# Performance work log

Measured on AMD Instinct MI355X. Metric: run time of the kernel, lower is better.

## Reference

```python
import jax, jax.numpy as jnp
import numpy as np

N_HEAD = 16
E = 1024
B, T = 2, 2048


def setup_inputs() -> dict:
    key = jax.random.key(0)
    ks = jax.random.split(key, 5)
    s = 1.0 / np.sqrt(E)
    return {
        "x": jax.random.normal(ks[0], (B, T, E), dtype=jnp.float32),
        "w_qkv": jax.random.normal(ks[1], (E, 3 * E), dtype=jnp.float32) * s,
        "b_qkv": jnp.zeros((3 * E,), dtype=jnp.float32),
        "w_proj": jax.random.normal(ks[2], (E, E), dtype=jnp.float32) * s,
        "b_proj": jnp.zeros((E,), dtype=jnp.float32),
    }


def reference(x, w_qkv, b_qkv, w_proj, b_proj):
    Bsz, Tlen, Emb = x.shape
    hd = Emb // N_HEAD
    qkv = x @ w_qkv + b_qkv  # [B, T, 3E]
    q, k, v = jnp.split(qkv, 3, axis=-1)
    # [B, H, T, hd]
    q = q.reshape(Bsz, Tlen, N_HEAD, hd).transpose(0, 2, 1, 3)
    k = k.reshape(Bsz, Tlen, N_HEAD, hd).transpose(0, 2, 1, 3)
    v = v.reshape(Bsz, Tlen, N_HEAD, hd).transpose(0, 2, 1, 3)
    scale = 1.0 / jnp.sqrt(jnp.asarray(hd, dtype=x.dtype))
    scores = jnp.einsum("bhqd,bhkd->bhqk", q, k) * scale  # [B, H, T, T]
    causal = jnp.tril(jnp.ones((Tlen, Tlen), dtype=bool))
    scores = jnp.where(causal, scores, jnp.asarray(-jnp.inf, dtype=scores.dtype))
    attn = jax.nn.softmax(scores, axis=-1)
    y = jnp.einsum("bhqk,bhkd->bhqd", attn, v)  # [B, H, T, hd]
    y = y.transpose(0, 2, 1, 3).reshape(Bsz, Tlen, Emb)
    return y @ w_proj + b_proj
```

## Files before the change

kernel.cpp:

```cpp
#include <hip/hip_runtime.h>
#include <hip/hip_bf16.h>

typedef __hip_bfloat16 bf16;
typedef __attribute__((ext_vector_type(8))) short sh8;
typedef __attribute__((ext_vector_type(4))) float f32x4;

#define BB 2
#define TT 2048
#define EE 1024
#define NH 16
#define HD 64
#define M_ROWS (BB * TT)
#define PPAD 72

__device__ __forceinline__ float b2f(bf16 v) { return __bfloat162float(v); }
__device__ __forceinline__ bf16 f2b(float v) { return __float2bfloat16(v); }
__device__ __forceinline__ unsigned short f2bu(float v) {
    union { bf16 b; unsigned short u; } x; x.b = f2b(v); return x.u;
}

__device__ __forceinline__ void gl2lds16(const bf16* g, bf16* l) {
    __builtin_amdgcn_global_load_lds(
        (__attribute__((address_space(1))) void*)g,
        (__attribute__((address_space(3))) void*)l, 16, 0, 0);
}

__global__ __launch_bounds__(256) void prep(
    const float* __restrict__ x, bf16* __restrict__ xb,
    const float* __restrict__ Wq, bf16* __restrict__ Wqt,
    const float* __restrict__ Wp, bf16* __restrict__ Wpt) {
    const int bid = blockIdx.x;
    if (bid < 4096) {
        const int i = bid * 256 + threadIdx.x;
        const float4 v = ((const float4*)x)[i];
        ushort4 u;
        u.x = f2bu(v.x); u.y = f2bu(v.y); u.z = f2bu(v.z); u.w = f2bu(v.w);
        ((ushort4*)xb)[i] = u;
        return;
    }
    __shared__ float Ld[64][65];
    const float* src; bf16* dst; int ncols, nc0, kr0;
    if (bid < 4096 + 768) {
        const int t = bid - 4096;
        src = Wq; dst = Wqt; ncols = 3072;
        nc0 = (t % 48) * 64; kr0 = (t / 48) * 64;
    } else {
        const int t = bid - 4096 - 768;
        src = Wp; dst = Wpt; ncols = 1024;
        nc0 = (t % 16) * 64; kr0 = (t / 16) * 64;
    }
#pragma unroll
    for (int i = 0; i < 16; ++i) {
        const int e = threadIdx.x + i * 256;
        Ld[e >> 6][e & 63] = src[(size_t)(kr0 + (e >> 6)) * ncols + nc0 + (e & 63)];
    }
    __syncthreads();
#pragma unroll
    for (int i = 0; i < 16; ++i) {
        const int e = threadIdx.x + i * 256;
        const int r2 = e & 63, c2 = e >> 6;
        dst[(size_t)(nc0 + c2) * EE + kr0 + r2] = f2b(Ld[r2][c2]);
    }
}

__device__ __forceinline__ void mfma_gemm_core(
    const bf16* __restrict__ A, const bf16* __restrict__ Bt,
    int m0, int n0, f32x4 acc[4][4], bf16* Al, bf16* Bl) {
    const int tid = threadIdx.x, w = tid >> 6, lane = tid & 63;
    const int li = lane & 15, quad = lane >> 4;
    const int wm = (w & 1) * 64, wn = (w >> 1) * 64;
    const int srow = w * 32 + (lane >> 3);
    const int scol = (lane & 7) * 8;

#pragma unroll
    for (int mt = 0; mt < 4; ++mt)
#pragma unroll
        for (int nt = 0; nt < 4; ++nt) acc[mt][nt] = (f32x4){0.f, 0.f, 0.f, 0.f};

    for (int k0 = 0; k0 < EE; k0 += 64) {
        __syncthreads();
#pragma unroll
        for (int j = 0; j < 4; ++j) {
            const int row = srow + j * 8;
            const int sk = scol ^ ((row & 7) * 8);
            gl2lds16(A  + (size_t)(m0 + row) * EE + k0 + sk, Al + row * 64 + scol);
            gl2lds16(Bt + (size_t)(n0 + row) * EE + k0 + sk, Bl + row * 64 + scol);
        }
        __syncthreads();
#pragma unroll
        for (int ks = 0; ks < 2; ++ks) {
            const int kof = (ks * 32 + quad * 8) ^ ((li & 7) * 8);
            sh8 af[4], bv[4];
#pragma unroll
            for (int mt = 0; mt < 4; ++mt)
                af[mt] = *(const sh8*)(Al + (wm + mt * 16 + li) * 64 + kof);
#pragma unroll
            for (int nt = 0; nt < 4; ++nt)
                bv[nt] = *(const sh8*)(Bl + (wn + nt * 16 + li) * 64 + kof);
#pragma unroll
            for (int mt = 0; mt < 4; ++mt)
#pragma unroll
                for (int nt = 0; nt < 4; ++nt)
                    acc[mt][nt] = __builtin_amdgcn_mfma_f32_16x16x32_bf16(
                        af[mt], bv[nt], acc[mt][nt], 0, 0, 0);
        }
    }
}

#define QBM 256
#define QBN 256
#define QBK 64
#define QNT (EE / QBK)

__global__ __launch_bounds__(512, 2) void gemm_qkv_8ph(
    const bf16* __restrict__ A, const bf16* __restrict__ Bt,
    const float* __restrict__ bias,
    bf16* __restrict__ Qb, bf16* __restrict__ Kb, bf16* __restrict__ Vb) {
    __shared__ bf16 Al[2][QBM * QBK];
    __shared__ bf16 Bl[2][QBN * QBK];

    const int tid  = threadIdx.x;
    const int lane = tid & 63;
    const int w    = tid >> 6;
    const int li   = lane & 15, quad = lane >> 4;
    const int wr   = w >> 2, wc = w & 3;
    const int wm   = wr << 7, wn = wc << 6;
    const int m0   = blockIdx.y << 8, n0 = blockIdx.x << 8;

    const int srow = tid >> 3;
    const int scol = (tid & 7) << 3;
    const int sg   = scol ^ ((srow & 7) << 3);
    const int swz  = (li & 7) << 3;
    const int kof0 = (quad << 3) ^ swz;
    const int kof1 = (32 + (quad << 3)) ^ swz;

    f32x4 acc[8][4];
#pragma unroll
    for (int m = 0; m < 8; ++m)
#pragma unroll
        for (int n = 0; n < 4; ++n) acc[m][n] = (f32x4){0.f, 0.f, 0.f, 0.f};

    sh8 ra[4][2];
    sh8 rb0[2][2];
    sh8 rb1[2][2];

#define QSTAGE_A(t, h) do {                                                    \
        const int _k0 = (t) * QBK; bf16* _lb = &Al[(t) & 1][0];                \
        _Pragma("unroll")                                                      \
        for (int _j = 0; _j < 2; ++_j) {                                       \
            const int _r = ((h) << 7) + (_j << 6) + srow;                      \
            gl2lds16(A + (size_t)(m0 + _r) * EE + _k0 + sg,                    \
                     _lb + _r * QBK + scol);                                   \
        }                                                                      \
    } while (0)

#define QSTAGE_B(t, h) do {                                                    \
        const int _k0 = (t) * QBK; bf16* _lb = &Bl[(t) & 1][0];                \
        _Pragma("unroll")                                                      \
        for (int _j = 0; _j < 2; ++_j) {                                       \
            const int _r = ((h) << 7) + (_j << 6) + srow;                      \
            gl2lds16(Bt + (size_t)(n0 + _r) * EE + _k0 + sg,                   \
                     _lb + _r * QBK + scol);                                   \
        }                                                                      \
    } while (0)

#define QLOAD_A(cb, a) do {                                                    \
        const bf16* _ab = &Al[cb][0];                                          \
        _Pragma("unroll")                                                      \
        for (int _m = 0; _m < 4; ++_m) {                                       \
            const int _row = wm + (((a) << 2) + _m) * 16 + li;                 \
            ra[_m][0] = *(const sh8*)(_ab + _row * QBK + kof0);                \
            ra[_m][1] = *(const sh8*)(_ab + _row * QBK + kof1);                \
        }                                                                      \
    } while (0)

#define QLOAD_B(cb, b, R) do {                                                 \
        const bf16* _bb = &Bl[cb][0];                                          \
        _Pragma("unroll")                                                      \
        for (int _n = 0; _n < 2; ++_n) {                                       \
            const int _row = wn + (((b) << 1) + _n) * 16 + li;                 \
            R[_n][0] = *(const sh8*)(_bb + _row * QBK + kof0);                 \
            R[_n][1] = *(const sh8*)(_bb + _row * QBK + kof1);                 \
        }                                                                      \
    } while (0)

#define QMFMA(a, b, R) do {                                                    \
        _Pragma("unroll")                                                      \
        for (int _m = 0; _m < 4; ++_m)                                         \
            _Pragma("unroll")                                                  \
            for (int _n = 0; _n < 2; ++_n) {                                   \
                acc[((a) << 2) + _m][((b) << 1) + _n] =                        \
                    __builtin_amdgcn_mfma_f32_16x16x32_bf16(                   \
                        ra[_m][0], R[_n][0],                                   \
                        acc[((a) << 2) + _m][((b) << 1) + _n], 0, 0, 0);       \
                acc[((a) << 2) + _m][((b) << 1) + _n] =                        \
                    __builtin_amdgcn_mfma_f32_16x16x32_bf16(                   \
                        ra[_m][1], R[_n][1],                                   \
                        acc[((a) << 2) + _m][((b) << 1) + _n], 0, 0, 0);       \
            }                                                                  \
    } while (0)

#define PH_MID() do { __builtin_amdgcn_s_barrier();                            \
        asm volatile("s_waitcnt lgkmcnt(0)" ::: "memory");                     \
        __builtin_amdgcn_s_setprio(1); } while (0)
#define PH_END() do { __builtin_amdgcn_s_setprio(0);                           \
        __builtin_amdgcn_s_barrier(); } while (0)
#define PH_END_VM4() do { __builtin_amdgcn_s_setprio(0);                       \
        asm volatile("s_waitcnt vmcnt(4)" ::: "memory");                       \
        __builtin_amdgcn_s_barrier(); } while (0)
#define PH_END_VM0() do { __builtin_amdgcn_s_setprio(0);                       \
        asm volatile("s_waitcnt vmcnt(0)" ::: "memory");                       \
        __builtin_amdgcn_s_barrier(); } while (0)

    QSTAGE_A(0, 0); QSTAGE_A(0, 1); QSTAGE_B(0, 0); QSTAGE_B(0, 1);
    QSTAGE_B(1, 0); QSTAGE_B(1, 1);
    asm volatile("s_waitcnt vmcnt(4)" ::: "memory");
    __builtin_amdgcn_s_barrier();

#pragma unroll 1
    for (int i = 0; i < QNT / 2 - 1; ++i) {
        const int ta = 2 * i + 1, tb = 2 * i + 2, tc = 2 * i + 3;
        QLOAD_A(0, 0); QLOAD_B(0, 0, rb0); QSTAGE_A(ta, 0);
        PH_MID(); QMFMA(0, 0, rb0); PH_END();
        QLOAD_B(0, 1, rb1); QSTAGE_A(ta, 1);
        PH_MID(); QMFMA(0, 1, rb1); PH_END();
        QLOAD_A(0, 1); QSTAGE_B(tb, 0);
        PH_MID(); QMFMA(1, 1, rb1); PH_END();
        QSTAGE_B(tb, 1);
        PH_MID(); QMFMA(1, 0, rb0); PH_END_VM4();
        QLOAD_A(1, 0); QLOAD_B(1, 0, rb0); QSTAGE_A(tb, 0);
        PH_MID(); QMFMA(0, 0, rb0); PH_END();
        QLOAD_B(1, 1, rb1); QSTAGE_A(tb, 1);
        PH_MID(); QMFMA(0, 1, rb1); PH_END();
        QLOAD_A(1, 1); QSTAGE_B(tc, 0);
        PH_MID(); QMFMA(1, 1, rb1); PH_END();
        QSTAGE_B(tc, 1);
        PH_MID(); QMFMA(1, 0, rb0); PH_END_VM4();
    }

    QLOAD_A(0, 0); QLOAD_B(0, 0, rb0); QSTAGE_A(QNT - 1, 0);
    PH_MID(); QMFMA(0, 0, rb0); PH_END();
    QLOAD_B(0, 1, rb1); QSTAGE_A(QNT - 1, 1);
    PH_MID(); QMFMA(0, 1, rb1); PH_END();
    QLOAD_A(0, 1);
    PH_MID(); QMFMA(1, 1, rb1); PH_END();
    PH_MID(); QMFMA(1, 0, rb0); PH_END_VM0();
    QLOAD_A(1, 0); QLOAD_B(1, 0, rb0);
    PH_MID(); QMFMA(0, 0, rb0); PH_END();
    QLOAD_B(1, 1, rb1);
    PH_MID(); QMFMA(0, 1, rb1); PH_END();
    QLOAD_A(1, 1);
    PH_MID(); QMFMA(1, 1, rb1); PH_END();
    PH_MID(); QMFMA(1, 0, rb0);
    __builtin_amdgcn_s_setprio(0);

#undef QSTAGE_A
#undef QSTAGE_B
#undef QLOAD_A
#undef QLOAD_B
#undef QMFMA
#undef PH_MID
#undef PH_END
#undef PH_END_VM4
#undef PH_END_VM0

    const int which = n0 >> 10;
#pragma unroll
    for (int nt = 0; nt < 4; ++nt) {
        const int n = n0 + wn + nt * 16 + li;
        const int hseg = n & 1023;
        const int h = hseg >> 6, d = hseg & 63;
        const float bv = bias[n];
        if (which == 2) {
#pragma unroll
            for (int mt = 0; mt < 8; ++mt) {
                const int mb = m0 + wm + mt * 16 + quad * 4;
                const int b = mb >> 11, t = mb & (TT - 1);
                ushort4 u;
                u.x = f2bu(acc[mt][nt][0] + bv);
                u.y = f2bu(acc[mt][nt][1] + bv);
                u.z = f2bu(acc[mt][nt][2] + bv);
                u.w = f2bu(acc[mt][nt][3] + bv);
                *(ushort4*)(Vb + ((size_t)((b * NH + h) * HD + d)) * TT + t) = u;
            }
        } else {
            bf16* dst = (which == 0) ? Qb : Kb;
            const float scl = (which == 0) ? 0.125f : 1.0f;
#pragma unroll
            for (int mt = 0; mt < 8; ++mt)
#pragma unroll
                for (int r = 0; r < 4; ++r) {
                    const int m = m0 + wm + mt * 16 + quad * 4 + r;
                    const int b = m >> 11, t = m & (TT - 1);
                    dst[((size_t)(b * NH + h) * TT + t) * HD + d] =
                        f2b((acc[mt][nt][r] + bv) * scl);
                }
        }
    }
}

__global__ __launch_bounds__(256) void gemm_proj_mfma(
    const bf16* __restrict__ A, const bf16* __restrict__ Bt,
    const float* __restrict__ bias, float* __restrict__ C) {
    __shared__ bf16 Al[128 * 64];
    __shared__ bf16 Bl[128 * 64];
    f32x4 acc[4][4];
    const int m0 = blockIdx.y * 128, n0 = blockIdx.x * 128;
    mfma_gemm_core(A, Bt, m0, n0, acc, Al, Bl);

    const int tid = threadIdx.x, w = tid >> 6, lane = tid & 63;
    const int li = lane & 15, quad = lane >> 4;
    const int wm = (w & 1) * 64, wn = (w >> 1) * 64;

#pragma unroll
    for (int nt = 0; nt < 4; ++nt) {
        const int n = n0 + wn + nt * 16 + li;
        const float bv = bias[n];
#pragma unroll
        for (int mt = 0; mt < 4; ++mt)
#pragma unroll
            for (int r = 0; r < 4; ++r) {
                const int m = m0 + wm + mt * 16 + quad * 4 + r;
                C[(size_t)m * EE + n] = acc[mt][nt][r] + bv;
            }
    }
}

__global__ __launch_bounds__(256) void attn_mfma(
    const bf16* __restrict__ Q, const bf16* __restrict__ K,
    const bf16* __restrict__ Vt, bf16* __restrict__ Y) {
    __shared__ bf16 Kl[2][64 * 64];
    __shared__ bf16 Vl[2][64 * 64];
    __shared__ bf16 Pl[4][16 * PPAD];

    const int tid  = threadIdx.x;
    const int w    = tid >> 6;
    const int lane = tid & 63;
    const int li   = lane & 15;
    const int quad = lane >> 4;
    const int swz  = (li & 7) * 8;
    const int idx  = blockIdx.x;
    const int qb   = 31 - (idx >> 5);
    const int bh   = idx & 31;
    const int q0   = qb << 6;
    const int qw0  = q0 + w * 16;

    const bf16* Qb = Q  + (size_t)bh * TT * HD;
    const bf16* Kb = K  + (size_t)bh * TT * HD;
    const bf16* Vb = Vt + (size_t)bh * HD * TT;

    sh8 qf0 = *(const sh8*)(Qb + (size_t)(qw0 + li) * HD + quad * 8);
    sh8 qf1 = *(const sh8*)(Qb + (size_t)(qw0 + li) * HD + 32 + quad * 8);

    f32x4 o[4];
#pragma unroll
    for (int nt = 0; nt < 4; ++nt) o[nt] = (f32x4){0.f, 0.f, 0.f, 0.f};
    float lacc = 0.f;

    const int l8 = lane >> 3, l7 = lane & 7;
    const int gcol = ((l7 ^ l8) * 8);

    const int ntiles = qb + 1;
#pragma unroll
    for (int c = 0; c < 2; ++c) {
        const int rb = w * 16 + c * 8;
        gl2lds16(Kb + (size_t)(rb + l8) * HD + gcol, &Kl[0][rb * 64]);
        gl2lds16(Vb + (size_t)(rb + l8) * TT + gcol, &Vl[0][rb * 64]);
    }

    for (int it = 0; it < ntiles; ++it) {
        const int cur = it & 1;
        __syncthreads();
        if (it + 1 < ntiles) {
            const int j1 = (it + 1) << 6;
            const int nxt = cur ^ 1;
#pragma unroll
            for (int c = 0; c < 2; ++c) {
                const int rb = w * 16 + c * 8;
                gl2lds16(Kb + (size_t)(j1 + rb + l8) * HD + gcol, &Kl[nxt][rb * 64]);
                gl2lds16(Vb + (size_t)(rb + l8) * TT + j1 + gcol, &Vl[nxt][rb * 64]);
            }
        }
        const bf16* kb = &Kl[cur][0];
        const bf16* vb = &Vl[cur][0];

        const bool diag = (it == ntiles - 1);
#pragma unroll
        for (int nt = 0; nt < 4; ++nt) {
            f32x4 a = (f32x4){0.f, 0.f, 0.f, 0.f};
            sh8 kf0 = *(const sh8*)(kb + (nt * 16 + li) * 64 + ((quad * 8) ^ swz));
            a = __builtin_amdgcn_mfma_f32_16x16x32_bf16(kf0, qf0, a, 0, 0, 0);
            sh8 kf1 = *(const sh8*)(kb + (nt * 16 + li) * 64 + ((32 + quad * 8) ^ swz));
            a = __builtin_amdgcn_mfma_f32_16x16x32_bf16(kf1, qf1, a, 0, 0, 0);

            ushort4 u;
            float p0, p1, p2, p3;
            if (diag) {
                const int keyb = q0 + nt * 16 + quad * 4;
                const int qg = qw0 + li;
                p0 = (keyb + 0 > qg) ? 0.f : __expf(a[0]);
                p1 = (keyb + 1 > qg) ? 0.f : __expf(a[1]);
                p2 = (keyb + 2 > qg) ? 0.f : __expf(a[2]);
                p3 = (keyb + 3 > qg) ? 0.f : __expf(a[3]);
            } else {
                p0 = __expf(a[0]); p1 = __expf(a[1]);
                p2 = __expf(a[2]); p3 = __expf(a[3]);
            }
            lacc += (p0 + p1) + (p2 + p3);
            u.x = f2bu(p0); u.y = f2bu(p1); u.z = f2bu(p2); u.w = f2bu(p3);
            *(ushort4*)(&Pl[w][li * PPAD + nt * 16 + quad * 4]) = u;
        }

#pragma unroll
        for (int ks = 0; ks < 2; ++ks) {
            sh8 pf = *(const sh8*)(&Pl[w][li * PPAD + ks * 32 + quad * 8]);
#pragma unroll
            for (int nt = 0; nt < 4; ++nt) {
                sh8 vf = *(const sh8*)(vb + (nt * 16 + li) * 64 +
                                       ((ks * 32 + quad * 8) ^ swz));
                o[nt] = __builtin_amdgcn_mfma_f32_16x16x32_bf16(pf, vf, o[nt], 0, 0, 0);
            }
        }
    }

    lacc += __shfl_xor(lacc, 16, 64);
    lacc += __shfl_xor(lacc, 32, 64);
    float rinv[4];
#pragma unroll
    for (int r = 0; r < 4; ++r)
        rinv[r] = 1.0f / __shfl(lacc, quad * 4 + r, 64);

    const int b = bh >> 4, h = bh & 15;
#pragma unroll
    for (int nt = 0; nt < 4; ++nt)
#pragma unroll
        for (int r = 0; r < 4; ++r) {
            const int q = qw0 + quad * 4 + r;
            Y[((size_t)(b * TT + q)) * EE + h * HD + nt * 16 + li] =
                f2b(o[nt][r] * rinv[r]);
        }
}

extern "C" void kernel_launch(void* const* d_in, const int* in_sizes, int n_in,
                              void* d_out, int out_size, void* d_ws, size_t ws_size,
                              hipStream_t stream) {
    const float* x      = (const float*)d_in[0];
    const float* w_qkv  = (const float*)d_in[1];
    const float* b_qkv  = (const float*)d_in[2];
    const float* w_proj = (const float*)d_in[3];
    const float* b_proj = (const float*)d_in[4];
    float* out = (float*)d_out;

    const size_t SZ = (size_t)M_ROWS * EE;
    bf16* Q   = (bf16*)d_ws;
    bf16* K   = Q + SZ;
    bf16* V   = K + SZ;
    bf16* XB  = V + SZ;
    bf16* WQT = XB + SZ;
    bf16* WPT = WQT + 3 * SZ / 4;
    bf16* Y   = XB;

    prep<<<dim3(4096 + 768 + 256), dim3(256), 0, stream>>>(
        x, XB, w_qkv, WQT, w_proj, WPT);

    gemm_qkv_8ph<<<dim3(12, 16), dim3(512), 0, stream>>>(XB, WQT, b_qkv, Q, K, V);

    attn_mfma<<<dim3((TT / 64) * (BB * NH)), dim3(256), 0, stream>>>(Q, K, V, Y);

    gemm_proj_mfma<<<dim3(8, 32), dim3(256), 0, stream>>>(Y, WPT, b_proj, out);
}
```

Measured before the change: 180.7 us.

## Split long causal attention rows across two blocks with a combine kernel

```diff
diff --git a/kernel.cpp b/kernel.cpp
--- a/kernel.cpp
+++ b/kernel.cpp
@@ -328,7 +328,8 @@
 
 __global__ __launch_bounds__(256) void attn_mfma(
     const bf16* __restrict__ Q, const bf16* __restrict__ K,
-    const bf16* __restrict__ Vt, bf16* __restrict__ Y) {
+    const bf16* __restrict__ Vt, bf16* __restrict__ Y,
+    float* __restrict__ Ow, float* __restrict__ lw) {
     __shared__ bf16 Kl[2][64 * 64];
     __shared__ bf16 Vl[2][64 * 64];
     __shared__ bf16 Pl[4][16 * PPAD];
@@ -339,11 +340,28 @@
     const int li   = lane & 15;
     const int quad = lane >> 4;
     const int swz  = (li & 7) * 8;
-    const int idx  = blockIdx.x;
-    const int qb   = 31 - (idx >> 5);
-    const int bh   = idx & 31;
-    const int q0   = qb << 6;
-    const int qw0  = q0 + w * 16;
+
+    const int idx = blockIdx.x;
+    int bh, qb, it0, it1;
+    bool split;
+    if (idx < 1024) {
+        split = true;
+        const int u = idx >> 1, s = idx & 1;
+        bh = u & 31;
+        qb = 31 - (u >> 5);
+        const int ntt = qb + 1;
+        const int h0 = ntt >> 1;
+        it0 = s ? h0 : 0;
+        it1 = s ? ntt : h0;
+    } else {
+        split = false;
+        const int i2 = idx - 1024;
+        bh = i2 & 31;
+        qb = 15 - (i2 >> 5);
+        it0 = 0; it1 = qb + 1;
+    }
+    const int q0  = qb << 6;
+    const int qw0 = q0 + w * 16;
 
     const bf16* Qb = Q  + (size_t)bh * TT * HD;
     const bf16* Kb = K  + (size_t)bh * TT * HD;
@@ -360,18 +378,18 @@
     const int l8 = lane >> 3, l7 = lane & 7;
     const int gcol = ((l7 ^ l8) * 8);
 
-    const int ntiles = qb + 1;
+    const int j00 = it0 << 6;
 #pragma unroll
     for (int c = 0; c < 2; ++c) {
         const int rb = w * 16 + c * 8;
-        gl2lds16(Kb + (size_t)(rb + l8) * HD + gcol, &Kl[0][rb * 64]);
-        gl2lds16(Vb + (size_t)(rb + l8) * TT + gcol, &Vl[0][rb * 64]);
-    }
-
-    for (int it = 0; it < ntiles; ++it) {
-        const int cur = it & 1;
+        gl2lds16(Kb + (size_t)(j00 + rb + l8) * HD + gcol, &Kl[0][rb * 64]);
+        gl2lds16(Vb + (size_t)(rb + l8) * TT + j00 + gcol, &Vl[0][rb * 64]);
+    }
+
+    for (int it = it0; it < it1; ++it) {
+        const int cur = (it - it0) & 1;
         __syncthreads();
-        if (it + 1 < ntiles) {
+        if (it + 1 < it1) {
             const int j1 = (it + 1) << 6;
             const int nxt = cur ^ 1;
 #pragma unroll
@@ -384,7 +402,7 @@
         const bf16* kb = &Kl[cur][0];
         const bf16* vb = &Vl[cur][0];
 
-        const bool diag = (it == ntiles - 1);
+        const bool diag = (it == qb);
 #pragma unroll
         for (int nt = 0; nt < 4; ++nt) {
             f32x4 a = (f32x4){0.f, 0.f, 0.f, 0.f};
@@ -396,7 +414,7 @@
             ushort4 u;
             float p0, p1, p2, p3;
             if (diag) {
-                const int keyb = q0 + nt * 16 + quad * 4;
+                const int keyb = (it << 6) + nt * 16 + quad * 4;
                 const int qg = qw0 + li;
                 p0 = (keyb + 0 > qg) ? 0.f : __expf(a[0]);
                 p1 = (keyb + 1 > qg) ? 0.f : __expf(a[1]);
@@ -425,6 +443,18 @@
 
     lacc += __shfl_xor(lacc, 16, 64);
     lacc += __shfl_xor(lacc, 32, 64);
+
+    if (split) {
+        float* Ob = Ow + (size_t)idx * 4096;
+#pragma unroll
+        for (int nt = 0; nt < 4; ++nt)
+#pragma unroll
+            for (int r = 0; r < 4; ++r)
+                Ob[(w * 16 + quad * 4 + r) * 64 + nt * 16 + li] = o[nt][r];
+        if (quad == 0) lw[(size_t)idx * 64 + w * 16 + li] = lacc;
+        return;
+    }
+
     float rinv[4];
 #pragma unroll
     for (int r = 0; r < 4; ++r)
@@ -439,6 +469,35 @@
             Y[((size_t)(b * TT + q)) * EE + h * HD + nt * 16 + li] =
                 f2b(o[nt][r] * rinv[r]);
         }
+}
+
+__global__ __launch_bounds__(256) void attn_combine(
+    const float* __restrict__ Ow, const float* __restrict__ lw,
+    bf16* __restrict__ Y) {
+    const int su = blockIdx.x;
+    const int qb = 31 - (su >> 5);
+    const int bh = su & 31;
+    const int b = bh >> 4, h = bh & 15;
+    const int t = threadIdx.x;
+    const int r = t >> 2;
+    const int dq = (t & 3) << 4;
+    const float* O0 = Ow + (size_t)(2 * su) * 4096 + r * 64 + dq;
+    const float* O1 = O0 + 4096;
+    const float inv = 1.0f / (lw[(size_t)(2 * su) * 64 + r] +
+                              lw[(size_t)(2 * su + 1) * 64 + r]);
+    const int q = (qb << 6) + r;
+    bf16* y = Y + ((size_t)(b * TT + q)) * EE + h * HD + dq;
+#pragma unroll
+    for (int j = 0; j < 4; ++j) {
+        const f32x4 a = *(const f32x4*)(O0 + j * 4);
+        const f32x4 c = *(const f32x4*)(O1 + j * 4);
+        ushort4 u;
+        u.x = f2bu((a[0] + c[0]) * inv);
+        u.y = f2bu((a[1] + c[1]) * inv);
+        u.z = f2bu((a[2] + c[2]) * inv);
+        u.w = f2bu((a[3] + c[3]) * inv);
+        *(ushort4*)(y + j * 4) = u;
+    }
 }
 
 extern "C" void kernel_launch(void* const* d_in, const int* in_sizes, int n_in,
@@ -459,13 +518,16 @@
     bf16* WQT = XB + SZ;
     bf16* WPT = WQT + 3 * SZ / 4;
     bf16* Y   = XB;
+    float* OW = (float*)(WPT + SZ / 4);
+    float* LW = OW + (size_t)1024 * 4096;
 
     prep<<<dim3(4096 + 768 + 256), dim3(256), 0, stream>>>(
         x, XB, w_qkv, WQT, w_proj, WPT);
 
     gemm_qkv_8ph<<<dim3(12, 16), dim3(512), 0, stream>>>(XB, WQT, b_qkv, Q, K, V);
 
-    attn_mfma<<<dim3((TT / 64) * (BB * NH)), dim3(256), 0, stream>>>(Q, K, V, Y);
+    attn_mfma<<<dim3(1536), dim3(256), 0, stream>>>(Q, K, V, Y, OW, LW);
+    attn_combine<<<dim3(512), dim3(256), 0, stream>>>(OW, LW, Y);
 
     gemm_proj_mfma<<<dim3(8, 32), dim3(256), 0, stream>>>(Y, WPT, b_proj, out);
 }
```

New measurement: 188.0 us. +4.0%, slower.

## Read K and V tiles directly from global memory instead of LDS double-buffering

Applied to the files above, without the earlier changes.

```diff
diff --git a/kernel.cpp b/kernel.cpp
--- a/kernel.cpp
+++ b/kernel.cpp
@@ -329,8 +329,6 @@
 __global__ __launch_bounds__(256) void attn_mfma(
     const bf16* __restrict__ Q, const bf16* __restrict__ K,
     const bf16* __restrict__ Vt, bf16* __restrict__ Y) {
-    __shared__ bf16 Kl[2][64 * 64];
-    __shared__ bf16 Vl[2][64 * 64];
     __shared__ bf16 Pl[4][16 * PPAD];
 
     const int tid  = threadIdx.x;
@@ -338,7 +336,6 @@
     const int lane = tid & 63;
     const int li   = lane & 15;
     const int quad = lane >> 4;
-    const int swz  = (li & 7) * 8;
     const int idx  = blockIdx.x;
     const int qb   = 31 - (idx >> 5);
     const int bh   = idx & 31;
@@ -357,46 +354,25 @@
     for (int nt = 0; nt < 4; ++nt) o[nt] = (f32x4){0.f, 0.f, 0.f, 0.f};
     float lacc = 0.f;
 
-    const int l8 = lane >> 3, l7 = lane & 7;
-    const int gcol = ((l7 ^ l8) * 8);
-
     const int ntiles = qb + 1;
-#pragma unroll
-    for (int c = 0; c < 2; ++c) {
-        const int rb = w * 16 + c * 8;
-        gl2lds16(Kb + (size_t)(rb + l8) * HD + gcol, &Kl[0][rb * 64]);
-        gl2lds16(Vb + (size_t)(rb + l8) * TT + gcol, &Vl[0][rb * 64]);
-    }
-
     for (int it = 0; it < ntiles; ++it) {
-        const int cur = it & 1;
-        __syncthreads();
-        if (it + 1 < ntiles) {
-            const int j1 = (it + 1) << 6;
-            const int nxt = cur ^ 1;
-#pragma unroll
-            for (int c = 0; c < 2; ++c) {
-                const int rb = w * 16 + c * 8;
-                gl2lds16(Kb + (size_t)(j1 + rb + l8) * HD + gcol, &Kl[nxt][rb * 64]);
-                gl2lds16(Vb + (size_t)(rb + l8) * TT + j1 + gcol, &Vl[nxt][rb * 64]);
-            }
-        }
-        const bf16* kb = &Kl[cur][0];
-        const bf16* vb = &Vl[cur][0];
-
-        const bool diag = (it == ntiles - 1);
+        const int j0 = it << 6;
+        const bf16* kt = Kb + (size_t)j0 * HD;
+        const bf16* vt = Vb + j0;
+        const bool diag = (it == qb);
+
 #pragma unroll
         for (int nt = 0; nt < 4; ++nt) {
             f32x4 a = (f32x4){0.f, 0.f, 0.f, 0.f};
-            sh8 kf0 = *(const sh8*)(kb + (nt * 16 + li) * 64 + ((quad * 8) ^ swz));
+            sh8 kf0 = *(const sh8*)(kt + (size_t)(nt * 16 + li) * HD + quad * 8);
+            sh8 kf1 = *(const sh8*)(kt + (size_t)(nt * 16 + li) * HD + 32 + quad * 8);
             a = __builtin_amdgcn_mfma_f32_16x16x32_bf16(kf0, qf0, a, 0, 0, 0);
-            sh8 kf1 = *(const sh8*)(kb + (nt * 16 + li) * 64 + ((32 + quad * 8) ^ swz));
             a = __builtin_amdgcn_mfma_f32_16x16x32_bf16(kf1, qf1, a, 0, 0, 0);
 
             ushort4 u;
             float p0, p1, p2, p3;
             if (diag) {
-                const int keyb = q0 + nt * 16 + quad * 4;
+                const int keyb = j0 + nt * 16 + quad * 4;
                 const int qg = qw0 + li;
                 p0 = (keyb + 0 > qg) ? 0.f : __expf(a[0]);
                 p1 = (keyb + 1 > qg) ? 0.f : __expf(a[1]);
@@ -416,8 +392,8 @@
             sh8 pf = *(const sh8*)(&Pl[w][li * PPAD + ks * 32 + quad * 8]);
 #pragma unroll
             for (int nt = 0; nt < 4; ++nt) {
-                sh8 vf = *(const sh8*)(vb + (nt * 16 + li) * 64 +
-                                       ((ks * 32 + quad * 8) ^ swz));
+                sh8 vf = *(const sh8*)(vt + (size_t)(nt * 16 + li) * TT +
+                                       ks * 32 + quad * 8);
                 o[nt] = __builtin_amdgcn_mfma_f32_16x16x32_bf16(pf, vf, o[nt], 0, 0, 0);
             }
         }
```

After: 275.8 us. +52.6%, slower.

## Shrink QKV GEMM N tile to 192 to fill all CUs

Applied to the files above, without the earlier changes.

```diff
diff --git a/kernel.cpp b/kernel.cpp
--- a/kernel.cpp
+++ b/kernel.cpp
@@ -108,7 +108,7 @@
 }
 
 #define QBM 256
-#define QBN 256
+#define QBN 192
 #define QBK 64
 #define QNT (EE / QBK)
 
@@ -124,8 +124,8 @@
     const int w    = tid >> 6;
     const int li   = lane & 15, quad = lane >> 4;
     const int wr   = w >> 2, wc = w & 3;
-    const int wm   = wr << 7, wn = wc << 6;
-    const int m0   = blockIdx.y << 8, n0 = blockIdx.x << 8;
+    const int wm   = wr << 7, wn = wc * 48;
+    const int m0   = blockIdx.y << 8, n0 = blockIdx.x * QBN;
 
     const int srow = tid >> 3;
     const int scol = (tid & 7) << 3;
@@ -134,15 +134,15 @@
     const int kof0 = (quad << 3) ^ swz;
     const int kof1 = (32 + (quad << 3)) ^ swz;
 
-    f32x4 acc[8][4];
+    f32x4 acc[8][3];
 #pragma unroll
     for (int m = 0; m < 8; ++m)
 #pragma unroll
-        for (int n = 0; n < 4; ++n) acc[m][n] = (f32x4){0.f, 0.f, 0.f, 0.f};
+        for (int n = 0; n < 3; ++n) acc[m][n] = (f32x4){0.f, 0.f, 0.f, 0.f};
 
     sh8 ra[4][2];
-    sh8 rb0[2][2];
-    sh8 rb1[2][2];
+    sh8 rb01[2][2];
+    sh8 rb2[2];
 
 #define QSTAGE_A(t, h) do {                                                    \
         const int _k0 = (t) * QBK; bf16* _lb = &Al[(t) & 1][0];                \
@@ -154,14 +154,11 @@
         }                                                                      \
     } while (0)
 
-#define QSTAGE_B(t, h) do {                                                    \
+#define QSTAGE_B(t, u) do {                                                    \
         const int _k0 = (t) * QBK; bf16* _lb = &Bl[(t) & 1][0];                \
-        _Pragma("unroll")                                                      \
-        for (int _j = 0; _j < 2; ++_j) {                                       \
-            const int _r = ((h) << 7) + (_j << 6) + srow;                      \
-            gl2lds16(Bt + (size_t)(n0 + _r) * EE + _k0 + sg,                   \
-                     _lb + _r * QBK + scol);                                   \
-        }                                                                      \
+        const int _r = ((u) << 6) + srow;                                      \
+        gl2lds16(Bt + (size_t)(n0 + _r) * EE + _k0 + sg,                       \
+                 _lb + _r * QBK + scol);                                       \
     } while (0)
 
 #define QLOAD_A(cb, a) do {                                                    \
@@ -174,30 +171,49 @@
         }                                                                      \
     } while (0)
 
-#define QLOAD_B(cb, b, R) do {                                                 \
+#define QLOAD_B01(cb) do {                                                     \
         const bf16* _bb = &Bl[cb][0];                                          \
         _Pragma("unroll")                                                      \
         for (int _n = 0; _n < 2; ++_n) {                                       \
-            const int _row = wn + (((b) << 1) + _n) * 16 + li;                 \
-            R[_n][0] = *(const sh8*)(_bb + _row * QBK + kof0);                 \
-            R[_n][1] = *(const sh8*)(_bb + _row * QBK + kof1);                 \
+            const int _row = wn + _n * 16 + li;                                \
+            rb01[_n][0] = *(const sh8*)(_bb + _row * QBK + kof0);              \
+            rb01[_n][1] = *(const sh8*)(_bb + _row * QBK + kof1);              \
         }                                                                      \
     } while (0)
 
-#define QMFMA(a, b, R) do {                                                    \
+#define QLOAD_B2(cb) do {                                                      \
+        const bf16* _bb = &Bl[cb][0];                                          \
+        const int _row = wn + 32 + li;                                         \
+        rb2[0] = *(const sh8*)(_bb + _row * QBK + kof0);                       \
+        rb2[1] = *(const sh8*)(_bb + _row * QBK + kof1);                       \
+    } while (0)
+
+#define QMFMA01(a) do {                                                        \
         _Pragma("unroll")                                                      \
         for (int _m = 0; _m < 4; ++_m)                                         \
             _Pragma("unroll")                                                  \
             for (int _n = 0; _n < 2; ++_n) {                                   \
-                acc[((a) << 2) + _m][((b) << 1) + _n] =                        \
+                acc[((a) << 2) + _m][_n] =                                     \
                     __builtin_amdgcn_mfma_f32_16x16x32_bf16(                   \
-                        ra[_m][0], R[_n][0],                                   \
-                        acc[((a) << 2) + _m][((b) << 1) + _n], 0, 0, 0);       \
-                acc[((a) << 2) + _m][((b) << 1) + _n] =                        \
+                        ra[_m][0], rb01[_n][0], acc[((a) << 2) + _m][_n],      \
+                        0, 0, 0);                                              \
+                acc[((a) << 2) + _m][_n] =                                     \
                     __builtin_amdgcn_mfma_f32_16x16x32_bf16(                   \
-                        ra[_m][1], R[_n][1],                                   \
-                        acc[((a) << 2) + _m][((b) << 1) + _n], 0, 0, 0);       \
+                        ra[_m][1], rb01[_n][1], acc[((a) << 2) + _m][_n],      \
+                        0, 0, 0);                                              \
             }                                                                  \
+    } while (0)
+
+#define QMFMA2(a) do {                                                         \
+        _Pragma("unroll")                                                      \
+        for (int _m = 0; _m < 4; ++_m) {                                       \
+            acc[((a) << 2) + _m][2] =                                          \
+                __builtin_amdgcn_mfma_f32_16x16x32_bf16(                       \
+                    ra[_m][0], rb2[0], acc[((a) << 2) + _m][2], 0, 0, 0);      \
+            acc[((a) << 2) + _m][2] =                                          \
+                __builtin_amdgcn_mfma_f32_16x16x32_bf16(                       \
+                    ra[_m][1], rb2[1], acc[((a) << 2) + _m][2], 0, 0, 0);      \
+        }                                                                      \
     } while (0)
 
 #define PH_MID() do { __builtin_amdgcn_s_barrier();                            \
@@ -205,69 +221,72 @@
         __builtin_amdgcn_s_setprio(1); } while (0)
 #define PH_END() do { __builtin_amdgcn_s_setprio(0);                           \
         __builtin_amdgcn_s_barrier(); } while (0)
-#define PH_END_VM4() do { __builtin_amdgcn_s_setprio(0);                       \
-        asm volatile("s_waitcnt vmcnt(4)" ::: "memory");                       \
+#define PH_END_VM3() do { __builtin_amdgcn_s_setprio(0);                       \
+        asm volatile("s_waitcnt vmcnt(3)" ::: "memory");                       \
         __builtin_amdgcn_s_barrier(); } while (0)
 #define PH_END_VM0() do { __builtin_amdgcn_s_setprio(0);                       \
         asm volatile("s_waitcnt vmcnt(0)" ::: "memory");                       \
         __builtin_amdgcn_s_barrier(); } while (0)
 
-    QSTAGE_A(0, 0); QSTAGE_A(0, 1); QSTAGE_B(0, 0); QSTAGE_B(0, 1);
-    QSTAGE_B(1, 0); QSTAGE_B(1, 1);
-    asm volatile("s_waitcnt vmcnt(4)" ::: "memory");
+    QSTAGE_A(0, 0); QSTAGE_A(0, 1);
+    QSTAGE_B(0, 0); QSTAGE_B(0, 1); QSTAGE_B(0, 2);
+    QSTAGE_B(1, 0); QSTAGE_B(1, 1); QSTAGE_B(1, 2);
+    asm volatile("s_waitcnt vmcnt(3)" ::: "memory");
     __builtin_amdgcn_s_barrier();
 
 #pragma unroll 1
     for (int i = 0; i < QNT / 2 - 1; ++i) {
         const int ta = 2 * i + 1, tb = 2 * i + 2, tc = 2 * i + 3;
-        QLOAD_A(0, 0); QLOAD_B(0, 0, rb0); QSTAGE_A(ta, 0);
-        PH_MID(); QMFMA(0, 0, rb0); PH_END();
-        QLOAD_B(0, 1, rb1); QSTAGE_A(ta, 1);
-        PH_MID(); QMFMA(0, 1, rb1); PH_END();
+        QLOAD_A(0, 0); QLOAD_B01(0); QSTAGE_A(ta, 0);
+        PH_MID(); QMFMA01(0); PH_END();
+        QLOAD_B2(0); QSTAGE_A(ta, 1);
+        PH_MID(); QMFMA2(0); PH_END();
         QLOAD_A(0, 1); QSTAGE_B(tb, 0);
-        PH_MID(); QMFMA(1, 1, rb1); PH_END();
-        QSTAGE_B(tb, 1);
-        PH_MID(); QMFMA(1, 0, rb0); PH_END_VM4();
-        QLOAD_A(1, 0); QLOAD_B(1, 0, rb0); QSTAGE_A(tb, 0);
-        PH_MID(); QMFMA(0, 0, rb0); PH_END();
-        QLOAD_B(1, 1, rb1); QSTAGE_A(tb, 1);
-        PH_MID(); QMFMA(0, 1, rb1); PH_END();
+        PH_MID(); QMFMA2(1); PH_END();
+        QSTAGE_B(tb, 1); QSTAGE_B(tb, 2);
+        PH_MID(); QMFMA01(1); PH_END_VM3();
+        QLOAD_A(1, 0); QLOAD_B01(1); QSTAGE_A(tb, 0);
+        PH_MID(); QMFMA01(0); PH_END();
+        QLOAD_B2(1); QSTAGE_A(tb, 1);
+        PH_MID(); QMFMA2(0); PH_END();
         QLOAD_A(1, 1); QSTAGE_B(tc, 0);
-        PH_MID(); QMFMA(1, 1, rb1); PH_END();
-        QSTAGE_B(tc, 1);
-        PH_MID(); QMFMA(1, 0, rb0); PH_END_VM4();
-    }
-
-    QLOAD_A(0, 0); QLOAD_B(0, 0, rb0); QSTAGE_A(QNT - 1, 0);
-    PH_MID(); QMFMA(0, 0, rb0); PH_END();
-    QLOAD_B(0, 1, rb1); QSTAGE_A(QNT - 1, 1);
-    PH_MID(); QMFMA(0, 1, rb1); PH_END();
+        PH_MID(); QMFMA2(1); PH_END();
+        QSTAGE_B(tc, 1); QSTAGE_B(tc, 2);
+        PH_MID(); QMFMA01(1); PH_END_VM3();
+    }
+
+    QLOAD_A(0, 0); QLOAD_B01(0); QSTAGE_A(QNT - 1, 0);
+    PH_MID(); QMFMA01(0); PH_END();
+    QLOAD_B2(0); QSTAGE_A(QNT - 1, 1);
+    PH_MID(); QMFMA2(0); PH_END();
     QLOAD_A(0, 1);
-    PH_MID(); QMFMA(1, 1, rb1); PH_END();
-    PH_MID(); QMFMA(1, 0, rb0); PH_END_VM0();
-    QLOAD_A(1, 0); QLOAD_B(1, 0, rb0);
-    PH_MID(); QMFMA(0, 0, rb0); PH_END();
-    QLOAD_B(1, 1, rb1);
-    PH_MID(); QMFMA(0, 1, rb1); PH_END();
+    PH_MID(); QMFMA2(1); PH_END();
+    PH_MID(); QMFMA01(1); PH_END_VM0();
+    QLOAD_A(1, 0); QLOAD_B01(1);
+    PH_MID(); QMFMA01(0); PH_END();
+    QLOAD_B2(1);
+    PH_MID(); QMFMA2(0); PH_END();
     QLOAD_A(1, 1);
-    PH_MID(); QMFMA(1, 1, rb1); PH_END();
-    PH_MID(); QMFMA(1, 0, rb0);
+    PH_MID(); QMFMA2(1); PH_END();
+    PH_MID(); QMFMA01(1);
     __builtin_amdgcn_s_setprio(0);
 
 #undef QSTAGE_A
 #undef QSTAGE_B
 #undef QLOAD_A
-#undef QLOAD_B
-#undef QMFMA
+#undef QLOAD_B01
+#undef QLOAD_B2
+#undef QMFMA01
+#undef QMFMA2
 #undef PH_MID
 #undef PH_END
-#undef PH_END_VM4
+#undef PH_END_VM3
 #undef PH_END_VM0
 
-    const int which = n0 >> 10;
-#pragma unroll
-    for (int nt = 0; nt < 4; ++nt) {
+#pragma unroll
+    for (int nt = 0; nt < 3; ++nt) {
         const int n = n0 + wn + nt * 16 + li;
+        const int which = n >> 10;
         const int hseg = n & 1023;
         const int h = hseg >> 6, d = hseg & 63;
         const float bv = bias[n];
@@ -463,7 +482,7 @@
     prep<<<dim3(4096 + 768 + 256), dim3(256), 0, stream>>>(
         x, XB, w_qkv, WQT, w_proj, WPT);
 
-    gemm_qkv_8ph<<<dim3(12, 16), dim3(512), 0, stream>>>(XB, WQT, b_qkv, Q, K, V);
+    gemm_qkv_8ph<<<dim3(16, 16), dim3(512), 0, stream>>>(XB, WQT, b_qkv, Q, K, V);
 
     attn_mfma<<<dim3((TT / 64) * (BB * NH)), dim3(256), 0, stream>>>(Q, K, V, Y);
 
```

Result: no change. 178.5 us (-1.2%).
